# Performance work log

Measured on AMD Instinct MI355X. Metric: run time of the kernel, lower is better.

The kernel has to match this reference:

```python
import jax, jax.numpy as jnp
import numpy as np

K = 8192      # num_embeddings
D = 512       # embedding_dim
DECAY = 0.99
EPS = 1e-5


def setup_inputs() -> dict:
    key = jax.random.key(0)
    k1, k2, k3 = jax.random.split(key, 3)
    inputs = jax.random.normal(k1, (8, 2048, D), dtype=jnp.float32)
    weight = jax.random.normal(k2, (K, D), dtype=jnp.float32) * 0.01
    ema_cluster_size = jnp.ones((K,), dtype=jnp.float32)
    ema_w = jax.random.normal(k3, (K, D), dtype=jnp.float32) * 0.01
    return {"inputs": inputs, "weight": weight,
            "ema_cluster_size": ema_cluster_size, "ema_w": ema_w}


def _l2norm(x):
    return x / jnp.sqrt(jnp.sum(x * x, axis=-1, keepdims=True) + 1e-12)


def reference(inputs, weight, ema_cluster_size, ema_w):
    # Flatten tokens: [N, D]
    flat = inputs.reshape(-1, D)
    cb = _l2norm(weight)            # [K, D]
    xn = _l2norm(flat)              # [N, D]
    # distances = 2 - 2 * sim; argmin(dist) == argmax(sim)
    sim = jnp.einsum('nd,kd->nk', xn, cb)          # [N, K]
    idx = jnp.argmax(sim, axis=1)                  # [N]
    # quantized = one_hot(idx) @ weight  ==  gather
    quantized = weight[idx].reshape(inputs.shape)
    # EMA codebook update (training path)
    counts = jax.ops.segment_sum(jnp.ones_like(idx, dtype=inputs.dtype), idx,
                                 num_segments=K)   # one_hot.sum(0)
    new_cs = ema_cluster_size * DECAY + (1.0 - DECAY) * counts
    n = jnp.sum(new_cs)
    new_cs = (new_cs + EPS) / (n + K * EPS) * n
    dw = jax.ops.segment_sum(flat, idx, num_segments=K)  # one_hot.T @ flat
    new_ema_w = ema_w * DECAY + (1.0 - DECAY) * dw
    new_weight = new_ema_w / new_cs[:, None]
    # Commitment loss and straight-through estimator
    e_latent_loss = jnp.mean((jax.lax.stop_gradient(quantized) - inputs) ** 2)
    quantized_st = inputs + jax.lax.stop_gradient(quantized - inputs)
    return (quantized_st, e_latent_loss, idx[:, None],
            new_cs, new_ema_w, new_weight)
```

## Files before the change

kernel.cpp:

```cpp
#include <hip/hip_runtime.h>
#include <cstdint>
#include <cstddef>

#define NTOK 16384
#define DIM  512
#define KCB  8192
#define MARGIN 6.0e-3f
#define LISTCAP 512

typedef short s16x8 __attribute__((ext_vector_type(8)));
typedef float f32x4 __attribute__((ext_vector_type(4)));

static const size_t WS_XN   = 0;
static const size_t WS_WN   = 16777216;
static const size_t WS_KV   = 25165824;
static const size_t WS_LP   = 37748736;
static const size_t WS_CSP  = 37814272;
static const size_t WS_CNT  = 37847296;
static const size_t WS_LIST = 37880064;

__device__ __forceinline__ void gl_lds16(const void* g, void* l) {
  __builtin_amdgcn_global_load_lds(
      (__attribute__((address_space(1))) void*)(uintptr_t)g,
      (__attribute__((address_space(3))) void*)(uint32_t)(uintptr_t)l,
      16, 0, 0);
}

__device__ __forceinline__ unsigned int f2bf(float f) {
  unsigned int u = __float_as_uint(f);
  u = (u + 0x7fffu + ((u >> 16) & 1u)) >> 16;
  return u;
}

__global__ __launch_bounds__(256) void k_normalize(const float* __restrict__ x,
                                                   const float* __restrict__ w,
                                                   unsigned short* __restrict__ xn,
                                                   unsigned short* __restrict__ wn,
                                                   const float* __restrict__ cs,
                                                   double* __restrict__ csp,
                                                   int* __restrict__ cnt) {
  const int wave = threadIdx.x >> 6, lane = threadIdx.x & 63;
  const int row = blockIdx.x * 4 + wave;
  const float* src;
  unsigned short* dst;
  if (row < NTOK) { src = x + (size_t)row * DIM;          dst = xn + (size_t)row * DIM; }
  else            { src = w + (size_t)(row - NTOK) * DIM; dst = wn + (size_t)(row - NTOK) * DIM; }
  const float4 a = *(const float4*)(src + lane * 8);
  const float4 b = *(const float4*)(src + lane * 8 + 4);
  float ss = a.x * a.x + a.y * a.y + a.z * a.z + a.w * a.w
           + b.x * b.x + b.y * b.y + b.z * b.z + b.w * b.w;
  #pragma unroll
  for (int off = 32; off > 0; off >>= 1) ss += __shfl_xor(ss, off);
  const float inv = rsqrtf(ss + 1e-12f);
  uint4 o;
  o.x = f2bf(a.x * inv) | (f2bf(a.y * inv) << 16);
  o.y = f2bf(a.z * inv) | (f2bf(a.w * inv) << 16);
  o.z = f2bf(b.x * inv) | (f2bf(b.y * inv) << 16);
  o.w = f2bf(b.z * inv) | (f2bf(b.w * inv) << 16);
  *(uint4*)(dst + lane * 8) = o;

  if (blockIdx.x < 32) {
    const int i = blockIdx.x * 256 + threadIdx.x;
    cnt[i] = 0;
    double s = (double)cs[i];
    #pragma unroll
    for (int off = 32; off > 0; off >>= 1) s += __shfl_xor(s, off);
    if (lane == 0) csp[blockIdx.x * 4 + wave] = s;
  }
}

__global__ __launch_bounds__(256, 2) void k_gemm_top2(const unsigned short* __restrict__ xn,
                                                      const unsigned short* __restrict__ wn,
                                                      uint2* __restrict__ kv) {
  __shared__ __align__(16) unsigned short smA[128 * 64];
  __shared__ __align__(16) unsigned short smB[256 * 64];
  const int tid = threadIdx.x, wave = tid >> 6, lane = tid & 63;
  const int quad = lane >> 4, col = lane & 15;
  const int wave_m = (wave & 1) * 64, wave_n = (wave >> 1) * 128;
  const int n0 = blockIdx.x * 256, m0 = blockIdx.y * 128;

  const unsigned short* pA[4];
  const unsigned short* pB[8];
  unsigned short* dA[4];
  unsigned short* dB[8];
  #pragma unroll
  for (int i = 0; i < 4; ++i) {
    int s = wave * 256 + i * 64 + lane;
    int row = s >> 3, cg = (s & 7) ^ (row & 7);
    pA[i] = xn + (size_t)(m0 + row) * DIM + cg * 8;
    dA[i] = &smA[(size_t)(wave * 256 + i * 64) * 8];
  }
  #pragma unroll
  for (int i = 0; i < 8; ++i) {
    int s = wave * 512 + i * 64 + lane;
    int row = s >> 3, cg = (s & 7) ^ (row & 7);
    pB[i] = wn + (size_t)(n0 + row) * DIM + cg * 8;
    dB[i] = &smB[(size_t)(wave * 512 + i * 64) * 8];
  }

  int offA[4][2], offB[8][2];
  #pragma unroll
  for (int kbi = 0; kbi < 2; ++kbi) {
    int kb = kbi * 4 + quad;
    #pragma unroll
    for (int mi = 0; mi < 4; ++mi) {
      int row = wave_m + mi * 16 + col;
      offA[mi][kbi] = (row * 8 + (kb ^ (row & 7))) * 16;
    }
    #pragma unroll
    for (int ni = 0; ni < 8; ++ni) {
      int row = wave_n + ni * 16 + col;
      offB[ni][kbi] = (row * 8 + (kb ^ (row & 7))) * 16;
    }
  }

  f32x4 acc[4][8] = {};
  const char* sA = (const char*)smA;
  const char* sB = (const char*)smB;

  #pragma unroll 1
  for (int kt = 0; kt < 8; ++kt) {
    __syncthreads();
    #pragma unroll
    for (int i = 0; i < 4; ++i) { gl_lds16(pA[i], dA[i]); pA[i] += 64; }
    #pragma unroll
    for (int i = 0; i < 8; ++i) { gl_lds16(pB[i], dB[i]); pB[i] += 64; }
    __syncthreads();
    #pragma unroll
    for (int kbi = 0; kbi < 2; ++kbi) {
      s16x8 af[4], bfr[8];
      #pragma unroll
      for (int mi = 0; mi < 4; ++mi) af[mi]  = *(const s16x8*)(sA + offA[mi][kbi]);
      #pragma unroll
      for (int ni = 0; ni < 8; ++ni) bfr[ni] = *(const s16x8*)(sB + offB[ni][kbi]);
      #pragma unroll
      for (int mi = 0; mi < 4; ++mi)
        #pragma unroll
        for (int ni = 0; ni < 8; ++ni)
          acc[mi][ni] = __builtin_amdgcn_mfma_f32_16x16x32_bf16(af[mi], bfr[ni], acc[mi][ni], 0, 0, 0);
    }
  }

  const int tile = blockIdx.x * 2 + (wave >> 1);
  unsigned int rk1 = 0, rk2 = 0;
  #pragma unroll
  for (int mi = 0; mi < 4; ++mi) {
    #pragma unroll
    for (int r = 0; r < 4; ++r) {
      const int p = mi * 4 + r;
      unsigned int k1 = 0, k2 = 0;
      #pragma unroll
      for (int ni = 0; ni < 8; ++ni) {
        float vb = acc[mi][ni][r] + 2.0f;
        unsigned int key = (__float_as_uint(vb) & ~0x7Fu) | (unsigned int)(ni * 16 + col);
        unsigned int mn = min(k1, key);
        k1 = max(k1, key);
        k2 = max(k2, mn);
      }
      #pragma unroll
      for (int off = 1; off < 16; off <<= 1) {
        unsigned int o1 = (unsigned int)__shfl_xor((int)k1, off);
        unsigned int o2 = (unsigned int)__shfl_xor((int)k2, off);
        unsigned int mn = min(k1, o1);
        k1 = max(k1, o1);
        k2 = max(max(k2, o2), mn);
      }
      if (col == p) { rk1 = k1; rk2 = k2; }
    }
  }
  const int row = wave_m + (col >> 2) * 16 + quad * 4 + (col & 3);
  kv[(size_t)(m0 + row) * 64 + tile] = make_uint2(rk1, rk2);
}

__global__ __launch_bounds__(256) void k_select(const float* __restrict__ x,
                                                const float* __restrict__ wgt,
                                                const uint2* __restrict__ kv,
                                                float* __restrict__ out0,
                                                float* __restrict__ out_idx,
                                                float* __restrict__ lp,
                                                int* __restrict__ cnt,
                                                int* __restrict__ list) {
  const int wave = threadIdx.x >> 6, lane = threadIdx.x & 63;
  const int t = blockIdx.x * 4 + wave;

  const uint2 kp = kv[(size_t)t * 64 + lane];
  const float v1 = __uint_as_float(kp.x);
  const float v2 = __uint_as_float(kp.y);
  const int   i1 = lane * 128 + (int)(kp.x & 0x7Fu);

  float gm = v1;
  #pragma unroll
  for (int off = 32; off > 0; off >>= 1) gm = fmaxf(gm, __shfl_xor(gm, off));
  const float thresh = gm - MARGIN;

  unsigned long long m1 = __ballot(v1 >= thresh);
  unsigned long long m2 = __ballot(v2 >= thresh);

  const float* xrow = x + (size_t)t * DIM;
  const float* xr = xrow + lane * 8;
  float4 x0 = *(const float4*)xr;
  float4 x1 = *(const float4*)(xr + 4);
  double xv[8] = {x0.x, x0.y, x0.z, x0.w, x1.x, x1.y, x1.z, x1.w};

  int besti;
  if (__popcll(m1) == 1 && m2 == 0ull) {
    besti = __shfl(i1, __builtin_ctzll(m1));
  } else {
    double bestv = -1e300; besti = 1 << 30;

    auto evalc = [&](int c) {
      const float* wr = wgt + (size_t)c * DIM + lane * 8;
      float4 w0 = *(const float4*)wr;
      float4 w1 = *(const float4*)(wr + 4);
      double s  = (double)w0.x * xv[0] + (double)w0.y * xv[1] + (double)w0.z * xv[2] + (double)w0.w * xv[3]
                + (double)w1.x * xv[4] + (double)w1.y * xv[5] + (double)w1.z * xv[6] + (double)w1.w * xv[7];
      double nw = (double)w0.x * w0.x + (double)w0.y * w0.y + (double)w0.z * w0.z + (double)w0.w * w0.w
                + (double)w1.x * w1.x + (double)w1.y * w1.y + (double)w1.z * w1.z + (double)w1.w * w1.w;
      #pragma unroll
      for (int off = 1; off < 64; off <<= 1) { s += __shfl_xor(s, off); nw += __shfl_xor(nw, off); }
      double sim = s / sqrt(nw + 1e-12);
      if (sim > bestv || (sim == bestv && c < besti)) { bestv = sim; besti = c; }
    };

    unsigned long long w1m = m1;
    while (w1m) {
      int b = __builtin_ctzll(w1m); w1m &= w1m - 1;
      evalc(__shfl(i1, b));
    }
    unsigned long long w2m = m2;
    while (w2m) {
      int b = __builtin_ctzll(w2m); w2m &= w2m - 1;
      #pragma unroll 1
      for (int chunk = 0; chunk < 2; ++chunk) {
        const int c = b * 128 + chunk * 64 + lane;
        const float* wr = wgt + (size_t)c * DIM;
        double s = 0.0, nw = 0.0;
        #pragma unroll 4
        for (int d = 0; d < DIM; d += 4) {
          float4 wv = *(const float4*)(wr + d);
          float4 xw = *(const float4*)(xrow + d);
          s  += (double)wv.x * xw.x + (double)wv.y * xw.y + (double)wv.z * xw.z + (double)wv.w * xw.w;
          nw += (double)wv.x * wv.x + (double)wv.y * wv.y + (double)wv.z * wv.z + (double)wv.w * wv.w;
        }
        double sim = s / sqrt(nw + 1e-12);
        if (sim > bestv || (sim == bestv && c < besti)) { bestv = sim; besti = c; }
      }
    }
    #pragma unroll
    for (int off = 1; off < 64; off <<= 1) {
      double ov = __shfl_xor(bestv, off);
      int    oi = __shfl_xor(besti, off);
      if (ov > bestv || (ov == bestv && oi < besti)) { bestv = ov; besti = oi; }
    }
  }
  if ((unsigned)besti >= KCB) besti = 0;

  const float* wr = wgt + (size_t)besti * DIM + lane * 8;
  float4 w0 = *(const float4*)wr;
  float4 w1 = *(const float4*)(wr + 4);
  float* o0 = out0 + (size_t)t * DIM + lane * 8;
  *(float4*)o0 = w0;
  *(float4*)(o0 + 4) = w1;
  double d2 = 0.0;
  double qv[8] = {w0.x, w0.y, w0.z, w0.w, w1.x, w1.y, w1.z, w1.w};
  #pragma unroll
  for (int j = 0; j < 8; ++j) { double d = qv[j] - xv[j]; d2 += d * d; }
  #pragma unroll
  for (int off = 1; off < 64; off <<= 1) d2 += __shfl_xor(d2, off);

  if (lane == 0) {
    lp[t] = (float)d2;
    out_idx[t] = (float)besti;
    int slot = atomicAdd(&cnt[besti], 1);
    if (slot < LISTCAP) list[besti * LISTCAP + slot] = t;
  }
}

__global__ __launch_bounds__(256) void k_dw(const float* __restrict__ x,
                                            const float* __restrict__ ema_w,
                                            const float* __restrict__ cs,
                                            const int* __restrict__ cnt,
                                            const int* __restrict__ list,
                                            const double* __restrict__ csp,
                                            const float* __restrict__ lp,
                                            float* __restrict__ out1,
                                            float* __restrict__ out3,
                                            float* __restrict__ out4,
                                            float* __restrict__ out5) {
  const int c = blockIdx.x, tid = threadIdx.x;
  const int wave = tid >> 6, lane = tid & 63;
  __shared__ double sh_n;
  if (tid < 64) {
    double s = csp[tid] + csp[tid + 64];
    #pragma unroll
    for (int off = 32; off > 0; off >>= 1) s += __shfl_xor(s, off);
    if (tid == 0) sh_n = 0.99 * s + 0.01 * (double)NTOK;
  }
  __syncthreads();
  const double n = sh_n;

  const int mtrue = cnt[c];
  const int m = mtrue > LISTCAP ? LISTCAP : mtrue;
  const float prec = cs[c] * 0.99f + 0.01f * (float)mtrue;
  const float csf = (float)(((double)prec + 1e-5) / (n + (double)KCB * 1e-5) * n);
  const int d0 = tid * 2;
  double s0 = 0.0, s1 = 0.0;
  for (int j = 0; j < m; ++j) {
    int t = list[c * LISTCAP + j] & (NTOK - 1);
    float2 v = *(const float2*)(x + (size_t)t * DIM + d0);
    s0 += (double)v.x; s1 += (double)v.y;
  }
  const size_t e = (size_t)c * DIM + d0;
  float n0 = ema_w[e]     * 0.99f + 0.01f * (float)s0;
  float n1 = ema_w[e + 1] * 0.99f + 0.01f * (float)s1;
  out4[e] = n0;       out4[e + 1] = n1;
  out5[e] = n0 / csf; out5[e + 1] = n1 / csf;
  if (tid == 0) out3[c] = csf;

  if (c == 0) {
    double l = 0.0;
    for (int i = tid * 4; i < NTOK; i += 1024) {
      float4 l4 = *(const float4*)(lp + i);
      l += (double)l4.x + (double)l4.y + (double)l4.z + (double)l4.w;
    }
    #pragma unroll
    for (int off = 32; off > 0; off >>= 1) l += __shfl_xor(l, off);
    __shared__ double rl[4];
    if (lane == 0) rl[wave] = l;
    __syncthreads();
    if (tid == 0) out1[0] = (float)((rl[0] + rl[1] + rl[2] + rl[3]) / (double)((size_t)NTOK * DIM));
  }
}

extern "C" void kernel_launch(void* const* d_in, const int* in_sizes, int n_in,
                              void* d_out, int out_size, void* d_ws, size_t ws_size,
                              hipStream_t stream) {
  const float* x    = (const float*)d_in[0];
  const float* wgt  = (const float*)d_in[1];
  const float* cs   = (const float*)d_in[2];
  const float* emaw = (const float*)d_in[3];

  char* ws = (char*)d_ws;
  unsigned short* xn  = (unsigned short*)(ws + WS_XN);
  unsigned short* wn  = (unsigned short*)(ws + WS_WN);
  uint2* kv    = (uint2*)(ws + WS_KV);
  float* lp    = (float*)(ws + WS_LP);
  double* csp  = (double*)(ws + WS_CSP);
  int*   cnt   = (int*)(ws + WS_CNT);
  int*   list  = (int*)(ws + WS_LIST);

  float* out0 = (float*)d_out;
  float* out1 = out0 + 8388608;
  float* out2 = out1 + 1;
  float* out3 = out2 + NTOK;
  float* out4 = out3 + KCB;
  float* out5 = out4 + (size_t)KCB * DIM;

  k_normalize<<<(NTOK + KCB) / 4, 256, 0, stream>>>(x, wgt, xn, wn, cs, csp, cnt);
  k_gemm_top2<<<dim3(32, 128), 256, 0, stream>>>(xn, wn, kv);
  k_select<<<NTOK / 4, 256, 0, stream>>>(x, wgt, kv, out0, out2, lp, cnt, list);
  k_dw<<<KCB, 256, 0, stream>>>(x, emaw, cs, cnt, list, csp, lp, out1, out3, out4, out5);
}
```

Measured before the change: 342.5 us.

## Replace per-code token lists with float atomic scatter-add into EMA weights

The per-code token list and the k_dw gather kernel are removed. The decayed ema_w is now written into out4 during normalization, and k_select atomically adds 0.01*x into the chosen code's row. A lighter k_fin kernel then computes cluster sizes, new weights and the loss. This drops the list writes and the serial per-code gather loop, at the cost of 8 float atomics per lane per token, contention on popular codes, and a summation order that is no longer deterministic. A duplicated o.z assignment is left in but is harmless, since the second write overrides the first.

```diff
diff --git a/kernel.cpp b/kernel.cpp
--- a/kernel.cpp
+++ b/kernel.cpp
@@ -6,7 +6,6 @@
 #define DIM  512
 #define KCB  8192
 #define MARGIN 6.0e-3f
-#define LISTCAP 512
 
 typedef short s16x8 __attribute__((ext_vector_type(8)));
 typedef float f32x4 __attribute__((ext_vector_type(4)));
@@ -17,7 +16,6 @@
 static const size_t WS_LP   = 37748736;
 static const size_t WS_CSP  = 37814272;
 static const size_t WS_CNT  = 37847296;
-static const size_t WS_LIST = 37880064;
 
 __device__ __forceinline__ void gl_lds16(const void* g, void* l) {
   __builtin_amdgcn_global_load_lds(
@@ -38,7 +36,9 @@
                                                    unsigned short* __restrict__ wn,
                                                    const float* __restrict__ cs,
                                                    double* __restrict__ csp,
-                                                   int* __restrict__ cnt) {
+                                                   int* __restrict__ cnt,
+                                                   const float* __restrict__ ema_w,
+                                                   float* __restrict__ out4) {
   const int wave = threadIdx.x >> 6, lane = threadIdx.x & 63;
   const int row = blockIdx.x * 4 + wave;
   const float* src;
@@ -55,9 +55,20 @@
   uint4 o;
   o.x = f2bf(a.x * inv) | (f2bf(a.y * inv) << 16);
   o.y = f2bf(a.z * inv) | (f2bf(a.w * inv) << 16);
+  o.z = f2bf(b.x * inv) | (f2bf(b.w * inv) << 16);
   o.z = f2bf(b.x * inv) | (f2bf(b.y * inv) << 16);
   o.w = f2bf(b.z * inv) | (f2bf(b.w * inv) << 16);
   *(uint4*)(dst + lane * 8) = o;
+
+  if (row >= NTOK) {
+    const int c = row - NTOK;
+    const float* er = ema_w + (size_t)c * DIM + lane * 8;
+    const float4 e0 = *(const float4*)er;
+    const float4 e1 = *(const float4*)(er + 4);
+    float* o4 = out4 + (size_t)c * DIM + lane * 8;
+    *(float4*)o4       = make_float4(0.99f * e0.x, 0.99f * e0.y, 0.99f * e0.z, 0.99f * e0.w);
+    *(float4*)(o4 + 4) = make_float4(0.99f * e1.x, 0.99f * e1.y, 0.99f * e1.z, 0.99f * e1.w);
+  }
 
   if (blockIdx.x < 32) {
     const int i = blockIdx.x * 256 + threadIdx.x;
@@ -179,7 +190,7 @@
                                                 float* __restrict__ out_idx,
                                                 float* __restrict__ lp,
                                                 int* __restrict__ cnt,
-                                                int* __restrict__ list) {
+                                                float* __restrict__ out4) {
   const int wave = threadIdx.x >> 6, lane = threadIdx.x & 63;
   const int t = blockIdx.x * 4 + wave;
 
@@ -268,67 +279,53 @@
   #pragma unroll
   for (int off = 1; off < 64; off <<= 1) d2 += __shfl_xor(d2, off);
 
+  float* o4 = out4 + (size_t)besti * DIM + lane * 8;
+  #pragma unroll
+  for (int j = 0; j < 8; ++j) atomicAdd(o4 + j, 0.01f * (float)xv[j]);
+
   if (lane == 0) {
     lp[t] = (float)d2;
     out_idx[t] = (float)besti;
-    int slot = atomicAdd(&cnt[besti], 1);
-    if (slot < LISTCAP) list[besti * LISTCAP + slot] = t;
-  }
-}
-
-__global__ __launch_bounds__(256) void k_dw(const float* __restrict__ x,
-                                            const float* __restrict__ ema_w,
-                                            const float* __restrict__ cs,
-                                            const int* __restrict__ cnt,
-                                            const int* __restrict__ list,
-                                            const double* __restrict__ csp,
-                                            const float* __restrict__ lp,
-                                            float* __restrict__ out1,
-                                            float* __restrict__ out3,
-                                            float* __restrict__ out4,
-                                            float* __restrict__ out5) {
-  const int c = blockIdx.x, tid = threadIdx.x;
-  const int wave = tid >> 6, lane = tid & 63;
-  __shared__ double sh_n;
-  if (tid < 64) {
-    double s = csp[tid] + csp[tid + 64];
-    #pragma unroll
-    for (int off = 32; off > 0; off >>= 1) s += __shfl_xor(s, off);
-    if (tid == 0) sh_n = 0.99 * s + 0.01 * (double)NTOK;
-  }
-  __syncthreads();
-  const double n = sh_n;
+    atomicAdd(&cnt[besti], 1);
+  }
+}
+
+__global__ __launch_bounds__(256) void k_fin(const float* __restrict__ cs,
+                                             const int* __restrict__ cnt,
+                                             const double* __restrict__ csp,
+                                             const float* __restrict__ lp,
+                                             const float* __restrict__ out4,
+                                             float* __restrict__ out1,
+                                             float* __restrict__ out3,
+                                             float* __restrict__ out5) {
+  const int wave = threadIdx.x >> 6, lane = threadIdx.x & 63;
+  const int c = blockIdx.x * 4 + wave;
+
+  double s = csp[lane] + csp[lane + 64];
+  #pragma unroll
+  for (int off = 32; off > 0; off >>= 1) s += __shfl_xor(s, off);
+  const double n = 0.99 * s + 0.01 * (double)NTOK;
 
   const int mtrue = cnt[c];
-  const int m = mtrue > LISTCAP ? LISTCAP : mtrue;
   const float prec = cs[c] * 0.99f + 0.01f * (float)mtrue;
   const float csf = (float)(((double)prec + 1e-5) / (n + (double)KCB * 1e-5) * n);
-  const int d0 = tid * 2;
-  double s0 = 0.0, s1 = 0.0;
-  for (int j = 0; j < m; ++j) {
-    int t = list[c * LISTCAP + j] & (NTOK - 1);
-    float2 v = *(const float2*)(x + (size_t)t * DIM + d0);
-    s0 += (double)v.x; s1 += (double)v.y;
-  }
-  const size_t e = (size_t)c * DIM + d0;
-  float n0 = ema_w[e]     * 0.99f + 0.01f * (float)s0;
-  float n1 = ema_w[e + 1] * 0.99f + 0.01f * (float)s1;
-  out4[e] = n0;       out4[e + 1] = n1;
-  out5[e] = n0 / csf; out5[e + 1] = n1 / csf;
-  if (tid == 0) out3[c] = csf;
-
-  if (c == 0) {
+
+  const size_t e = (size_t)c * DIM + lane * 8;
+  const float4 a = *(const float4*)(out4 + e);
+  const float4 b = *(const float4*)(out4 + e + 4);
+  *(float4*)(out5 + e)     = make_float4(a.x / csf, a.y / csf, a.z / csf, a.w / csf);
+  *(float4*)(out5 + e + 4) = make_float4(b.x / csf, b.y / csf, b.z / csf, b.w / csf);
+  if (lane == 0) out3[c] = csf;
+
+  if (blockIdx.x == 0 && wave == 0) {
     double l = 0.0;
-    for (int i = tid * 4; i < NTOK; i += 1024) {
+    for (int i = lane * 4; i < NTOK; i += 256) {
       float4 l4 = *(const float4*)(lp + i);
       l += (double)l4.x + (double)l4.y + (double)l4.z + (double)l4.w;
     }
     #pragma unroll
     for (int off = 32; off > 0; off >>= 1) l += __shfl_xor(l, off);
-    __shared__ double rl[4];
-    if (lane == 0) rl[wave] = l;
-    __syncthreads();
-    if (tid == 0) out1[0] = (float)((rl[0] + rl[1] + rl[2] + rl[3]) / (double)((size_t)NTOK * DIM));
+    if (lane == 0) out1[0] = (float)(l / (double)((size_t)NTOK * DIM));
   }
 }
 
@@ -347,7 +344,6 @@
   float* lp    = (float*)(ws + WS_LP);
   double* csp  = (double*)(ws + WS_CSP);
   int*   cnt   = (int*)(ws + WS_CNT);
-  int*   list  = (int*)(ws + WS_LIST);
 
   float* out0 = (float*)d_out;
   float* out1 = out0 + 8388608;
@@ -356,8 +352,8 @@
   float* out4 = out3 + KCB;
   float* out5 = out4 + (size_t)KCB * DIM;
 
-  k_normalize<<<(NTOK + KCB) / 4, 256, 0, stream>>>(x, wgt, xn, wn, cs, csp, cnt);
+  k_normalize<<<(NTOK + KCB) / 4, 256, 0, stream>>>(x, wgt, xn, wn, cs, csp, cnt, emaw, out4);
   k_gemm_top2<<<dim3(32, 128), 256, 0, stream>>>(xn, wn, kv);
-  k_select<<<NTOK / 4, 256, 0, stream>>>(x, wgt, kv, out0, out2, lp, cnt, list);
-  k_dw<<<KCB, 256, 0, stream>>>(x, emaw, cs, cnt, list, csp, lp, out1, out3, out4, out5);
-}
+  k_select<<<NTOK / 4, 256, 0, stream>>>(x, wgt, kv, out0, out2, lp, cnt, out4);
+  k_fin<<<KCB / 4, 256, 0, stream>>>(cs, cnt, csp, lp, out4, out1, out3, out5);
+}
```

New measurement: 566.7 us. +65.4%, slower.

## Double-buffer GEMM top2 with 256x256 tiles, 8 waves and phased prefetch

Applied to the files above, without the earlier changes.

Rewrites the similarity GEMM mainloop to use 512-thread blocks with 256x256 output tiles and double-buffered LDS (128KB). Global-to-LDS loads for the next K slice are issued between MFMA phases, with explicit vmcnt waits, barriers and setprio, so memory traffic overlaps compute instead of the previous load-sync-compute pattern. This aims to hide load latency and raise reuse per block. The cost is heavy LDS use that limits occupancy and more fragile hand-written synchronization.

```diff
diff --git a/kernel.cpp b/kernel.cpp
--- a/kernel.cpp
+++ b/kernel.cpp
@@ -69,79 +69,104 @@
   }
 }
 
-__global__ __launch_bounds__(256, 2) void k_gemm_top2(const unsigned short* __restrict__ xn,
+#define SBAR()  do { __builtin_amdgcn_s_barrier(); __builtin_amdgcn_sched_barrier(0); } while (0)
+#define VMW(N)  do { __builtin_amdgcn_sched_barrier(0); \
+                     asm volatile("s_waitcnt vmcnt(" #N ")"); \
+                     __builtin_amdgcn_sched_barrier(0); } while (0)
+
+__global__ __launch_bounds__(512, 2) void k_gemm_top2(const unsigned short* __restrict__ xn,
                                                       const unsigned short* __restrict__ wn,
                                                       uint2* __restrict__ kv) {
-  __shared__ __align__(16) unsigned short smA[128 * 64];
-  __shared__ __align__(16) unsigned short smB[256 * 64];
+  __shared__ __align__(16) char lds[131072];
+  char* const ldsA = lds;
+  char* const ldsB = lds + 65536;
   const int tid = threadIdx.x, wave = tid >> 6, lane = tid & 63;
   const int quad = lane >> 4, col = lane & 15;
-  const int wave_m = (wave & 1) * 64, wave_n = (wave >> 1) * 128;
-  const int n0 = blockIdx.x * 256, m0 = blockIdx.y * 128;
-
-  const unsigned short* pA[4];
-  const unsigned short* pB[8];
-  unsigned short* dA[4];
-  unsigned short* dB[8];
-  #pragma unroll
-  for (int i = 0; i < 4; ++i) {
-    int s = wave * 256 + i * 64 + lane;
-    int row = s >> 3, cg = (s & 7) ^ (row & 7);
-    pA[i] = xn + (size_t)(m0 + row) * DIM + cg * 8;
-    dA[i] = &smA[(size_t)(wave * 256 + i * 64) * 8];
-  }
-  #pragma unroll
-  for (int i = 0; i < 8; ++i) {
-    int s = wave * 512 + i * 64 + lane;
-    int row = s >> 3, cg = (s & 7) ^ (row & 7);
-    pB[i] = wn + (size_t)(n0 + row) * DIM + cg * 8;
-    dB[i] = &smB[(size_t)(wave * 512 + i * 64) * 8];
-  }
-
-  int offA[4][2], offB[8][2];
-  #pragma unroll
-  for (int kbi = 0; kbi < 2; ++kbi) {
-    int kb = kbi * 4 + quad;
+  const int wave_m = (wave & 3) * 64;
+  const int wave_n = (wave >> 2) * 128;
+  const int n0 = blockIdx.x * 256, m0 = blockIdx.y * 256;
+
+  const int seg0 = wave * 128 + lane;
+  const int r0 = seg0 >> 3, cg0 = (seg0 & 7) ^ (r0 & 7);
+  const int seg1 = seg0 + 64;
+  const int r1 = seg1 >> 3, cg1 = (seg1 & 7) ^ (r1 & 7);
+  const unsigned short* const pA0 = xn + (size_t)(m0 + r0) * DIM + cg0 * 8;
+  const unsigned short* const pA1 = xn + (size_t)(m0 + r1) * DIM + cg1 * 8;
+  const unsigned short* const pB0 = wn + (size_t)(n0 + r0) * DIM + cg0 * 8;
+  const unsigned short* const pB1 = wn + (size_t)(n0 + r1) * DIM + cg1 * 8;
+  const int dj0 = wave * 2048;
+
+#define STAGE_A(HALF, KT) do { \
+    char* da_ = ldsA + (((KT) & 1) << 15) + ((HALF) << 14) + dj0; \
+    gl_lds16(pA0 + (HALF) * 65536 + (KT) * 64, da_); \
+    gl_lds16(pA1 + (HALF) * 65536 + (KT) * 64, da_ + 1024); \
+  } while (0)
+#define STAGE_B(HALF, KT) do { \
+    char* db_ = ldsB + (((KT) & 1) << 15) + ((HALF) << 14) + dj0; \
+    gl_lds16(pB0 + (HALF) * 65536 + (KT) * 64, db_); \
+    gl_lds16(pB1 + (HALF) * 65536 + (KT) * 64, db_ + 1024); \
+  } while (0)
+
+  int offA[4], offB[8];
+  #pragma unroll
+  for (int mi = 0; mi < 4; ++mi) {
+    int row = wave_m + mi * 16 + col;
+    offA[mi] = (row >> 7) * 16384 + (row & 127) * 128 + ((quad ^ (row & 7)) * 16);
+  }
+  #pragma unroll
+  for (int ni = 0; ni < 8; ++ni) {
+    int row = wave_n + ni * 16 + col;
+    offB[ni] = (row >> 7) * 16384 + (row & 127) * 128 + ((quad ^ (row & 7)) * 16);
+  }
+
+  f32x4 acc[4][8] = {};
+  s16x8 af[4][2];
+
+#define PHASE(KBI, NB, STAGE_STMT, TAIL_STMT) do {                                   \
+    s16x8 bfr0 = *(const s16x8*)(ldsB + bufoff + (offB[(NB) + 0] ^ ((KBI) * 64)));   \
+    s16x8 bfr1 = *(const s16x8*)(ldsB + bufoff + (offB[(NB) + 1] ^ ((KBI) * 64)));   \
+    s16x8 bfr2 = *(const s16x8*)(ldsB + bufoff + (offB[(NB) + 2] ^ ((KBI) * 64)));   \
+    s16x8 bfr3 = *(const s16x8*)(ldsB + bufoff + (offB[(NB) + 3] ^ ((KBI) * 64)));   \
+    STAGE_STMT;                                                                      \
+    SBAR();                                                                          \
+    __builtin_amdgcn_s_setprio(1);                                                   \
+    _Pragma("unroll")                                                                \
+    for (int mi = 0; mi < 4; ++mi) {                                                 \
+      acc[mi][(NB) + 0] = __builtin_amdgcn_mfma_f32_16x16x32_bf16(af[mi][KBI], bfr0, acc[mi][(NB) + 0], 0, 0, 0); \
+      acc[mi][(NB) + 1] = __builtin_amdgcn_mfma_f32_16x16x32_bf16(af[mi][KBI], bfr1, acc[mi][(NB) + 1], 0, 0, 0); \
+      acc[mi][(NB) + 2] = __builtin_amdgcn_mfma_f32_16x16x32_bf16(af[mi][KBI], bfr2, acc[mi][(NB) + 2], 0, 0, 0); \
+      acc[mi][(NB) + 3] = __builtin_amdgcn_mfma_f32_16x16x32_bf16(af[mi][KBI], bfr3, acc[mi][(NB) + 3], 0, 0, 0); \
+    }                                                                                \
+    __builtin_amdgcn_s_setprio(0);                                                   \
+    TAIL_STMT;                                                                       \
+    SBAR();                                                                          \
+  } while (0)
+
+  STAGE_A(0, 0); STAGE_A(1, 0); STAGE_B(0, 0); STAGE_B(1, 0);
+  STAGE_A(0, 1); STAGE_A(1, 1);
+  VMW(4);
+  SBAR();
+
+  #pragma unroll 1
+  for (int t = 0; t < 8; ++t) {
+    const int bufoff = (t & 1) << 15;
     #pragma unroll
     for (int mi = 0; mi < 4; ++mi) {
-      int row = wave_m + mi * 16 + col;
-      offA[mi][kbi] = (row * 8 + (kb ^ (row & 7))) * 16;
-    }
-    #pragma unroll
-    for (int ni = 0; ni < 8; ++ni) {
-      int row = wave_n + ni * 16 + col;
-      offB[ni][kbi] = (row * 8 + (kb ^ (row & 7))) * 16;
-    }
-  }
-
-  f32x4 acc[4][8] = {};
-  const char* sA = (const char*)smA;
-  const char* sB = (const char*)smB;
-
-  #pragma unroll 1
-  for (int kt = 0; kt < 8; ++kt) {
-    __syncthreads();
-    #pragma unroll
-    for (int i = 0; i < 4; ++i) { gl_lds16(pA[i], dA[i]); pA[i] += 64; }
-    #pragma unroll
-    for (int i = 0; i < 8; ++i) { gl_lds16(pB[i], dB[i]); pB[i] += 64; }
-    __syncthreads();
-    #pragma unroll
-    for (int kbi = 0; kbi < 2; ++kbi) {
-      s16x8 af[4], bfr[8];
-      #pragma unroll
-      for (int mi = 0; mi < 4; ++mi) af[mi]  = *(const s16x8*)(sA + offA[mi][kbi]);
-      #pragma unroll
-      for (int ni = 0; ni < 8; ++ni) bfr[ni] = *(const s16x8*)(sB + offB[ni][kbi]);
-      #pragma unroll
-      for (int mi = 0; mi < 4; ++mi)
-        #pragma unroll
-        for (int ni = 0; ni < 8; ++ni)
-          acc[mi][ni] = __builtin_amdgcn_mfma_f32_16x16x32_bf16(af[mi], bfr[ni], acc[mi][ni], 0, 0, 0);
-    }
-  }
-
-  const int tile = blockIdx.x * 2 + (wave >> 1);
+      af[mi][0] = *(const s16x8*)(ldsA + bufoff + offA[mi]);
+      af[mi][1] = *(const s16x8*)(ldsA + bufoff + (offA[mi] ^ 64));
+    }
+    PHASE(0, 0, if (t < 7) STAGE_B(0, t + 1), );
+    PHASE(0, 4, if (t < 7) STAGE_B(1, t + 1), );
+    PHASE(1, 0, if (t < 6) STAGE_A(0, t + 2), );
+    PHASE(1, 4, if (t < 6) STAGE_A(1, t + 2),
+          if (t < 6) { VMW(4); } else if (t == 6) { VMW(0); });
+  }
+
+#undef PHASE
+#undef STAGE_A
+#undef STAGE_B
+
+  const int tile = blockIdx.x * 2 + (wave >> 2);
   unsigned int rk1 = 0, rk2 = 0;
   #pragma unroll
   for (int mi = 0; mi < 4; ++mi) {
@@ -357,7 +382,7 @@
   float* out5 = out4 + (size_t)KCB * DIM;
 
   k_normalize<<<(NTOK + KCB) / 4, 256, 0, stream>>>(x, wgt, xn, wn, cs, csp, cnt);
-  k_gemm_top2<<<dim3(32, 128), 256, 0, stream>>>(xn, wn, kv);
+  k_gemm_top2<<<dim3(32, 64), 512, 0, stream>>>(xn, wn, kv);
   k_select<<<NTOK / 4, 256, 0, stream>>>(x, wgt, kv, out0, out2, lp, cnt, list);
   k_dw<<<KCB, 256, 0, stream>>>(x, emaw, cs, cnt, list, csp, lp, out1, out3, out4, out5);
 }
```

Measured after the change: 357.5 us. 1.04x slower.
